# Performance work log

Hardware: AMD Instinct MI355X
Metric: run time of the kernel (lower is better)

Reference implementation:

```python
import jax, jax.numpy as jnp
import numpy as np

D_MODEL = 1024
NUM_HEADS = 16
HEAD_DIM = D_MODEL // NUM_HEADS
B, S = 2, 2048
EPS = 1e-8


def setup_inputs() -> dict:
    key = jax.random.key(0)
    ks = jax.random.split(key, 9)
    sc = 1.0 / np.sqrt(D_MODEL)
    return {
        "x": jax.random.normal(ks[0], (B, S, D_MODEL), jnp.float32),
        "wq": jax.random.normal(ks[1], (D_MODEL, D_MODEL), jnp.float32) * sc,
        "bq": jax.random.normal(ks[2], (D_MODEL,), jnp.float32) * 0.01,
        "wk": jax.random.normal(ks[3], (D_MODEL, D_MODEL), jnp.float32) * sc,
        "bk": jax.random.normal(ks[4], (D_MODEL,), jnp.float32) * 0.01,
        "wv": jax.random.normal(ks[5], (D_MODEL, D_MODEL), jnp.float32) * sc,
        "bv": jax.random.normal(ks[6], (D_MODEL,), jnp.float32) * 0.01,
        "wo": jax.random.normal(ks[7], (D_MODEL, D_MODEL), jnp.float32) * sc,
        "bo": jax.random.normal(ks[8], (D_MODEL,), jnp.float32) * 0.01,
    }


def reference(x, wq, bq, wk, bk, wv, bv, wo, bo):
    b, s, d = x.shape
    h, hd = NUM_HEADS, HEAD_DIM
    # projections (torch Linear: y = x W^T + b); reshape to [b, h, s, hd]
    def proj(w, bias):
        return (jnp.einsum('bsd,ed->bse', x, w) + bias).reshape(b, s, h, hd).transpose(0, 2, 1, 3)
    q = proj(wq, bq)
    k = proj(wk, bk)
    v = proj(wv, bv)
    scores = jnp.einsum('bhqd,bhkd->bhqk', q, k) / np.sqrt(hd)
    attn = jax.nn.softmax(scores, axis=-1)
    o = jnp.einsum('bhqk,bhkd->bhqd', attn, v)  # [b, h, s, hd]
    # per-position, per-head Gram-Schmidt exclusion: remove component of o[i]
    # along v[i] (the loop in the original is independent over positions)
    v_norm_sq = jnp.sum(v * v, axis=-1, keepdims=True)          # [b,h,s,1]
    align = jnp.sum(o * v, axis=-1, keepdims=True) / (v_norm_sq + EPS)
    o = o - align * v
    o = o.transpose(0, 2, 1, 3).reshape(b, s, d)
    return jnp.einsum('bsd,ed->bse', o, wo) + bo
```

## Files before the change

kernel.cpp:

```cpp
#include <hip/hip_runtime.h>
#include <stdint.h>

#define SEQ 2048
#define NTOK 4096
#define DM 1024

typedef __bf16 bf16x8 __attribute__((ext_vector_type(8)));
typedef __bf16 bf16x4 __attribute__((ext_vector_type(4)));
typedef float f32x4 __attribute__((ext_vector_type(4)));

__device__ __forceinline__ unsigned short f2bf(float f) {
  union { float f; unsigned u; } v; v.f = f;
  return (unsigned short)((v.u + 0x7fffu + ((v.u >> 16) & 1u)) >> 16);
}
__device__ __forceinline__ float bf2f(unsigned short s) {
  union { unsigned u; float f; } v; v.u = ((unsigned)s) << 16; return v.f;
}
__device__ __forceinline__ unsigned pkbf(float a, float b) {
  union { float f; unsigned u; } x, y; x.f = a; y.f = b;
  return __builtin_amdgcn_perm(y.u + 0x8000u, x.u + 0x8000u, 0x07060302u);
}

__device__ __forceinline__ void async16(const unsigned short* g, unsigned short* l) {
  __builtin_amdgcn_global_load_lds(
      (const __attribute__((address_space(1))) void*)g,
      (__attribute__((address_space(3))) void*)l, 16, 0, 0);
}

__global__ __launch_bounds__(256) void cast_all(
    const float* __restrict__ x, const float* __restrict__ wq,
    const float* __restrict__ wk, const float* __restrict__ wv,
    const float* __restrict__ wo, unsigned short* __restrict__ dst) {
  size_t i = ((size_t)blockIdx.x * 256 + threadIdx.x) * 4;
  const float* src; size_t off;
  if (i < (size_t)NTOK * DM) { src = x; off = i; }
  else {
    size_t j = i - (size_t)NTOK * DM;
    int s = (int)(j >> 20);
    src = (s == 0) ? wq : (s == 1) ? wk : (s == 2) ? wv : wo;
    off = j & 1048575u;
  }
  float4 f = *(const float4*)(src + off);
  ushort4 o;
  o.x = f2bf(f.x); o.y = f2bf(f.y); o.z = f2bf(f.z); o.w = f2bf(f.w);
  *(ushort4*)(dst + i) = o;
}

__device__ __forceinline__ void gemm128_bk64(
    const unsigned short* __restrict__ A, const unsigned short* __restrict__ Bw,
    int m0, int n0, f32x4 acc[4][4], unsigned short* As, unsigned short* Bs) {
  const int tid = threadIdx.x, lane = tid & 63, w = tid >> 6;
  const int wm = (w >> 1) * 64, wn = (w & 1) * 64;
  const int quad = lane >> 4, l16 = lane & 15, sel = l16 & 7;
  const int srow = tid >> 3;
  const int sc = ((tid & 7) ^ (srow & 7)) << 3;

  for (int kt = 0; kt < 1024; kt += 64) {
    __syncthreads();
#pragma unroll
    for (int c = 0; c < 4; ++c) {
      const int row = c * 32 + srow;
      async16(A + (size_t)(m0 + row) * 1024 + kt + sc, As + c * 2048 + tid * 8);
      async16(Bw + (size_t)(n0 + row) * 1024 + kt + sc, Bs + c * 2048 + tid * 8);
    }
    __syncthreads();
#pragma unroll
    for (int ks = 0; ks < 2; ++ks) {
      bf16x8 af[4], bf[4];
#pragma unroll
      for (int i = 0; i < 4; ++i)
        af[i] = *(const bf16x8*)(As + (wm + i * 16 + l16) * 64 + (((ks * 4 + quad) ^ sel) << 3));
#pragma unroll
      for (int j = 0; j < 4; ++j)
        bf[j] = *(const bf16x8*)(Bs + (wn + j * 16 + l16) * 64 + (((ks * 4 + quad) ^ sel) << 3));
#pragma unroll
      for (int i = 0; i < 4; ++i)
#pragma unroll
        for (int j = 0; j < 4; ++j)
          acc[i][j] = __builtin_amdgcn_mfma_f32_16x16x32_bf16(af[i], bf[j], acc[i][j], 0, 0, 0);
    }
  }
}

__global__ __launch_bounds__(256) void qkv_gemm(
    const unsigned short* __restrict__ xb,
    const unsigned short* __restrict__ wqb, const unsigned short* __restrict__ wkb,
    const unsigned short* __restrict__ wvb,
    const float* __restrict__ bq, const float* __restrict__ bk, const float* __restrict__ bv,
    unsigned short* __restrict__ Q, unsigned short* __restrict__ Kd,
    unsigned short* __restrict__ Vt) {
  __shared__ unsigned short As[128 * 64], Bs[128 * 64];
  const int gx = blockIdx.x;
  const int kind = gx >> 8;
  const int rr = gx & 255;
  const int tok = 4 * (rr & 7) + ((rr >> 3) & 3);
  const int oth = rr >> 5;
  const unsigned short* A; const unsigned short* Bw;
  int m0, n0;
  if (kind == 2) { A = wvb; Bw = xb; m0 = oth * 128; n0 = tok * 128; }
  else { A = xb; Bw = kind ? wkb : wqb; m0 = tok * 128; n0 = oth * 128; }

  f32x4 acc[4][4];
#pragma unroll
  for (int i = 0; i < 4; ++i)
#pragma unroll
    for (int j = 0; j < 4; ++j) { f32x4 z = {0.f, 0.f, 0.f, 0.f}; acc[i][j] = z; }
  gemm128_bk64(A, Bw, m0, n0, acc, As, Bs);

  const int lane = threadIdx.x & 63, w = threadIdx.x >> 6;
  const int quad = lane >> 4, l16 = lane & 15;
  const int wm = (w >> 1) * 64, wn = (w & 1) * 64;

  if (kind == 2) {
#pragma unroll
    for (int i = 0; i < 4; ++i)
#pragma unroll
      for (int j = 0; j < 4; ++j) {
        const int n = n0 + wn + j * 16 + l16;
        const int tb = n >> 11, s = n & 2047;
#pragma unroll
        for (int r = 0; r < 4; ++r) {
          const int m = m0 + wm + i * 16 + quad * 4 + r;
          const int h = m >> 6, d = m & 63;
          Vt[((size_t)(tb * 16 + h) * 64 + d) * SEQ + s] = f2bf(acc[i][j][r] + bv[m]);
        }
      }
  } else {
    const float* bias = (kind == 0) ? bq : bk;
    const float scale = (kind == 0) ? 0.180336880f : 1.0f;
#pragma unroll
    for (int i = 0; i < 4; ++i)
#pragma unroll
      for (int j = 0; j < 4; ++j) {
        const int col = n0 + wn + j * 16 + l16;
        const float bb = bias[col];
        const int h = col >> 6, d = col & 63;
#pragma unroll
        for (int r = 0; r < 4; ++r) {
          const int m = m0 + wm + i * 16 + quad * 4 + r;
          const int b = m >> 11, s = m & 2047;
          const int bh = b * 16 + h;
          const unsigned short val = f2bf((acc[i][j][r] + bb) * scale);
          if (kind == 0) Q[((size_t)bh * SEQ + s) * 64 + d] = val;
          else           Kd[((size_t)bh * SEQ + s) * 64 + d] = val;
        }
      }
  }
}

__global__ __launch_bounds__(256, 2) void attn_kernel(
    const unsigned short* __restrict__ Q, const unsigned short* __restrict__ Kd,
    const unsigned short* __restrict__ Vt,
    unsigned short* __restrict__ Op, float* __restrict__ Lp) {
  __shared__ unsigned short KV[4][4096];
  const int gx = blockIdx.x;
  const int xcd = gx & 7;
  const int idx = gx >> 3;
  const int bh  = xcd * 4 + (idx & 3);
  const int ksl = (idx >> 2) & 1;
  const int q0  = (idx >> 3) * 256;
  const int ks0 = ksl << 10;
  const int tid = threadIdx.x, lane = tid & 63, w = tid >> 6;
  const int quad = lane >> 4, l16 = lane & 15;
  const unsigned short* Qp = Q + (size_t)bh * SEQ * 64;
  const unsigned short* Kp = Kd + (size_t)bh * SEQ * 64;
  const unsigned short* Vp = Vt + (size_t)bh * 64 * SEQ;
  const int srow = tid >> 3;
  const int sc = ((tid & 7) ^ (srow & 7)) << 3;

#pragma unroll
  for (int c = 0; c < 8; ++c)
    async16(Qp + (size_t)(q0 + c * 32 + srow) * 64 + sc,
            KV[c >> 1] + (c & 1) * 2048 + tid * 8);
  __syncthreads();

  const int sel = l16 & 7;
  const unsigned short* Qsrc = KV[w];
  bf16x8 bQ[4][2];
#pragma unroll
  for (int qq = 0; qq < 4; ++qq) {
    const int qrow = qq * 16 + l16;
#pragma unroll
    for (int hh = 0; hh < 2; ++hh)
      bQ[qq][hh] = *(const bf16x8*)(Qsrc + qrow * 64 + (((hh * 4 + quad) ^ sel) << 3));
  }
  __syncthreads();

  async16(Kp + (size_t)(ks0 + srow) * 64 + sc, KV[0] + tid * 8);
  async16(Kp + (size_t)(ks0 + 32 + srow) * 64 + sc, KV[0] + 2048 + tid * 8);
  async16(Vp + (size_t)srow * SEQ + ks0 + sc, KV[2] + tid * 8);
  async16(Vp + (size_t)(32 + srow) * SEQ + ks0 + sc, KV[2] + 2048 + tid * 8);

  union { unsigned short u[8]; bf16x8 v; } one8;
#pragma unroll
  for (int t = 0; t < 8; ++t) one8.u[t] = 0x3F80;
  const bf16x8 aOnes = one8.v;

  f32x4 o_acc[4][4];
  f32x4 l_acc[4];
  const f32x4 zinit = {-12.f, -12.f, -12.f, -12.f};
#pragma unroll
  for (int qq = 0; qq < 4; ++qq) {
    f32x4 z = {0.f, 0.f, 0.f, 0.f};
    l_acc[qq] = z;
#pragma unroll
    for (int dt = 0; dt < 4; ++dt) o_acc[qq][dt] = z;
  }

  for (int it = 0; it < 16; ++it) {
    const int cur = it & 1;
    __syncthreads();
    if (it + 1 < 16) {
      const int kt = ks0 + (it + 1) * 64, nb = (it + 1) & 1;
      async16(Kp + (size_t)(kt + srow) * 64 + sc, KV[nb] + tid * 8);
      async16(Kp + (size_t)(kt + 32 + srow) * 64 + sc, KV[nb] + 2048 + tid * 8);
      async16(Vp + (size_t)srow * SEQ + kt + sc, KV[2 + nb] + tid * 8);
      async16(Vp + (size_t)(32 + srow) * SEQ + kt + sc, KV[2 + nb] + 2048 + tid * 8);
    }
    const unsigned short* Ks = KV[cur];
    const unsigned short* Vs = KV[2 + cur];

    bf16x8 bP[4][2];
#pragma unroll
    for (int kk = 0; kk < 4; ++kk) {
      const int krow = kk * 16 + l16;
      bf16x8 a0 = *(const bf16x8*)(Ks + krow * 64 + ((quad ^ sel) << 3));
      bf16x8 a1 = *(const bf16x8*)(Ks + krow * 64 + (((4 + quad) ^ sel) << 3));
#pragma unroll
      for (int qq = 0; qq < 4; ++qq) {
        f32x4 z = __builtin_amdgcn_mfma_f32_16x16x32_bf16(a0, bQ[qq][0], zinit, 0, 0, 0);
        z = __builtin_amdgcn_mfma_f32_16x16x32_bf16(a1, bQ[qq][1], z, 0, 0, 0);
#pragma unroll
        for (int r = 0; r < 4; ++r) z[r] = __builtin_amdgcn_exp2f(z[r]);
        unsigned lo = pkbf(z[0], z[1]);
        unsigned hi = pkbf(z[2], z[3]);
        union { unsigned d[4]; bf16x8 v; } pk;
        pk.v = bP[qq][kk >> 1];
        pk.d[(kk & 1) * 2] = lo;
        pk.d[(kk & 1) * 2 + 1] = hi;
        bP[qq][kk >> 1] = pk.v;
      }
    }

#pragma unroll
    for (int qq = 0; qq < 4; ++qq)
#pragma unroll
      for (int G = 0; G < 2; ++G)
        l_acc[qq] = __builtin_amdgcn_mfma_f32_16x16x32_bf16(aOnes, bP[qq][G], l_acc[qq], 0, 0, 0);

#pragma unroll
    for (int dt = 0; dt < 4; ++dt) {
      const unsigned short* vbase = Vs + (dt * 16 + l16) * 64;
      const int inner = (quad & 1) * 4;
#pragma unroll
      for (int G = 0; G < 2; ++G) {
        const int c0 = 4 * G + (quad >> 1);
        bf16x4 lo = *(const bf16x4*)(vbase + ((c0 ^ sel) << 3) + inner);
        bf16x4 hi = *(const bf16x4*)(vbase + (((c0 + 2) ^ sel) << 3) + inner);
        bf16x8 aV = __builtin_shufflevector(lo, hi, 0, 1, 2, 3, 4, 5, 6, 7);
#pragma unroll
        for (int qq = 0; qq < 4; ++qq)
          o_acc[qq][dt] = __builtin_amdgcn_mfma_f32_16x16x32_bf16(aV, bP[qq][G], o_acc[qq][dt], 0, 0, 0);
      }
    }
  }

  const size_t sb = (size_t)(ksl * 32 + bh);
#pragma unroll
  for (int qq = 0; qq < 4; ++qq) {
    const int qg = q0 + w * 64 + qq * 16 + l16;
#pragma unroll
    for (int dt = 0; dt < 4; ++dt)
#pragma unroll
      for (int r = 0; r < 4; ++r) {
        const int d = dt * 16 + quad * 4 + r;
        Op[(sb * 64 + d) * SEQ + qg] = f2bf(o_acc[qq][dt][r]);
      }
    if (quad == 0) Lp[sb * SEQ + qg] = l_acc[qq][0];
  }
}

__global__ __launch_bounds__(128) void combine_kernel(
    const unsigned short* __restrict__ Op, const float* __restrict__ Lp,
    const unsigned short* __restrict__ Vt, unsigned short* __restrict__ O) {
  const int bh = blockIdx.y;
  const int q = blockIdx.x * 128 + threadIdx.x;
  const size_t QC = (size_t)32 * SEQ;
  const size_t idx = (size_t)bh * SEQ + q;
  const float inv = 1.0f / (Lp[idx] + Lp[QC + idx]);
  const unsigned short* O1 = Op + (size_t)bh * 64 * SEQ + q;
  const unsigned short* O2 = O1 + QC * 64;
  const unsigned short* Vp = Vt + (size_t)bh * 64 * SEQ + q;
  float o64[64];
  float ov = 0.f, vv = 0.f;
#pragma unroll
  for (int d = 0; d < 64; ++d) {
    const float o = (bf2f(O1[(size_t)d * SEQ]) + bf2f(O2[(size_t)d * SEQ])) * inv;
    const float v = bf2f(Vp[(size_t)d * SEQ]);
    o64[d] = o; ov += o * v; vv += v * v;
  }
  const float align = ov / (vv + 1e-8f);
  const int b = bh >> 4, h = bh & 15;
  unsigned short* dst = O + (size_t)(b * SEQ + q) * DM + h * 64;
#pragma unroll
  for (int d = 0; d < 64; d += 2) {
    const float a0 = o64[d]     - align * bf2f(Vp[(size_t)d * SEQ]);
    const float a1 = o64[d + 1] - align * bf2f(Vp[(size_t)(d + 1) * SEQ]);
    *(unsigned*)(dst + d) = pkbf(a0, a1);
  }
}

__global__ __launch_bounds__(256) void out_gemm(
    const unsigned short* __restrict__ Ob, const unsigned short* __restrict__ wob,
    const float* __restrict__ bo, float* __restrict__ out) {
  __shared__ unsigned short As[64 * 64], Bs[128 * 64];
  const int m0 = blockIdx.y * 64, n0 = blockIdx.x * 128;
  const int tid = threadIdx.x, lane = tid & 63, w = tid >> 6;
  const int wm = (w >> 1) * 32, wn = (w & 1) * 64;
  const int quad = lane >> 4, l16 = lane & 15, sel = l16 & 7;
  const int srow = tid >> 3;
  const int sc = ((tid & 7) ^ (srow & 7)) << 3;
  f32x4 acc[2][4];
#pragma unroll
  for (int i = 0; i < 2; ++i)
#pragma unroll
    for (int j = 0; j < 4; ++j) { f32x4 z = {0.f, 0.f, 0.f, 0.f}; acc[i][j] = z; }

  for (int kt = 0; kt < 1024; kt += 64) {
    __syncthreads();
#pragma unroll
    for (int c = 0; c < 2; ++c) {
      const int row = c * 32 + srow;
      async16(Ob + (size_t)(m0 + row) * 1024 + kt + sc, As + c * 2048 + tid * 8);
    }
#pragma unroll
    for (int c = 0; c < 4; ++c) {
      const int row = c * 32 + srow;
      async16(wob + (size_t)(n0 + row) * 1024 + kt + sc, Bs + c * 2048 + tid * 8);
    }
    __syncthreads();
#pragma unroll
    for (int ks = 0; ks < 2; ++ks) {
      bf16x8 af[2], bf[4];
#pragma unroll
      for (int i = 0; i < 2; ++i)
        af[i] = *(const bf16x8*)(As + (wm + i * 16 + l16) * 64 + (((ks * 4 + quad) ^ sel) << 3));
#pragma unroll
      for (int j = 0; j < 4; ++j)
        bf[j] = *(const bf16x8*)(Bs + (wn + j * 16 + l16) * 64 + (((ks * 4 + quad) ^ sel) << 3));
#pragma unroll
      for (int i = 0; i < 2; ++i)
#pragma unroll
        for (int j = 0; j < 4; ++j)
          acc[i][j] = __builtin_amdgcn_mfma_f32_16x16x32_bf16(af[i], bf[j], acc[i][j], 0, 0, 0);
    }
  }

#pragma unroll
  for (int i = 0; i < 2; ++i)
#pragma unroll
    for (int j = 0; j < 4; ++j) {
      const int col = n0 + wn + j * 16 + l16;
      const float bb = bo[col];
#pragma unroll
      for (int r = 0; r < 4; ++r) {
        const int m = m0 + wm + i * 16 + quad * 4 + r;
        out[(size_t)m * DM + col] = acc[i][j][r] + bb;
      }
    }
}

extern "C" void kernel_launch(void* const* d_in, const int* in_sizes, int n_in,
                              void* d_out, int out_size, void* d_ws, size_t ws_size,
                              hipStream_t stream) {
  const float* x  = (const float*)d_in[0];
  const float* wq = (const float*)d_in[1];
  const float* bq = (const float*)d_in[2];
  const float* wk = (const float*)d_in[3];
  const float* bk = (const float*)d_in[4];
  const float* wv = (const float*)d_in[5];
  const float* bv = (const float*)d_in[6];
  const float* wo = (const float*)d_in[7];
  const float* bo = (const float*)d_in[8];
  float* out = (float*)d_out;
  (void)in_sizes; (void)n_in; (void)out_size; (void)ws_size;

  unsigned short* ws  = (unsigned short*)d_ws;
  unsigned short* xb  = ws;
  unsigned short* wqb = xb + (size_t)NTOK * DM;
  unsigned short* wkb = wqb + (size_t)DM * DM;
  unsigned short* wvb = wkb + (size_t)DM * DM;
  unsigned short* wob = wvb + (size_t)DM * DM;
  unsigned short* Qb  = wob + (size_t)DM * DM;
  unsigned short* Kb  = Qb + (size_t)NTOK * DM;
  unsigned short* Vtb = Kb + (size_t)NTOK * DM;
  unsigned short* Ob  = Vtb + (size_t)NTOK * DM;
  unsigned short* Opb = Ob + (size_t)NTOK * DM;
  float* Lpw = (float*)(Opb + (size_t)2 * 32 * 64 * SEQ);

  cast_all<<<8192, 256, 0, stream>>>(x, wq, wk, wv, wo, ws);
  qkv_gemm<<<768, 256, 0, stream>>>(xb, wqb, wkb, wvb, bq, bk, bv, Qb, Kb, Vtb);
  attn_kernel<<<512, 256, 0, stream>>>(Qb, Kb, Vtb, Opb, Lpw);
  combine_kernel<<<dim3(16, 32), 128, 0, stream>>>(Opb, Lpw, Vtb, Ob);
  out_gemm<<<dim3(8, 64), 256, 0, stream>>>(Ob, wob, bo, out);
}
```

Before: 194.1 us.

## Triple-buffer GEMM LDS tiles with async prefetch and vmcnt-gated barriers

Replaces the synchronous load-then-compute loop in the QKV and output GEMMs with a shared templated pipeline. It uses a 3-slot LDS ring of BK=32 half-tiles and prefetches two stages ahead with global_load_lds. Each step waits on a partial vmcnt before a single barrier, so the next tiles load while MFMAs run. This is meant to hide global memory latency and halve the barrier count per k-step. The cost is more LDS use and hand-tuned waitcnt values that must match the number of issued loads, which is fragile.

Result: faster. 185.7 us (-4.3%).

```diff
diff --git a/kernel.cpp b/kernel.cpp
--- a/kernel.cpp
+++ b/kernel.cpp
@@ -46,50 +46,91 @@
   *(ushort4*)(dst + i) = o;
 }
 
-__device__ __forceinline__ void gemm128_bk64(
+
+template<int MI>
+__device__ __forceinline__ void stage_half(
     const unsigned short* __restrict__ A, const unsigned short* __restrict__ Bw,
-    int m0, int n0, f32x4 acc[4][4], unsigned short* As, unsigned short* Bs) {
+    int m0, int n0, int kt, unsigned short* As, unsigned short* Bs) {
+  const int tid = threadIdx.x;
+  const int r = tid >> 2, c = tid & 3;
+#pragma unroll
+  for (int b = 0; b < MI / 2; ++b) {
+    const int row = b * 64 + r;
+    async16(A + (size_t)(m0 + row) * 1024 + kt + ((c ^ (row & 3)) << 3),
+            As + row * 32 + c * 8);
+  }
+#pragma unroll
+  for (int b = 0; b < 2; ++b) {
+    const int row = b * 64 + r;
+    async16(Bw + (size_t)(n0 + row) * 1024 + kt + ((c ^ (row & 3)) << 3),
+            Bs + row * 32 + c * 8);
+  }
+}
+
+__device__ __forceinline__ void pipe_bar0() {
+  asm volatile("s_waitcnt vmcnt(0)\ns_barrier" ::: "memory");
+}
+template<int MI>
+__device__ __forceinline__ void pipe_barN() {
+  if constexpr (MI == 4) asm volatile("s_waitcnt vmcnt(4)\ns_barrier" ::: "memory");
+  else                   asm volatile("s_waitcnt vmcnt(3)\ns_barrier" ::: "memory");
+}
+
+template<int MI>
+__device__ __forceinline__ void gemm_pipe(
+    const unsigned short* __restrict__ A, const unsigned short* __restrict__ Bw,
+    int m0, int n0, f32x4 (&acc)[MI][4],
+    unsigned short* AsBase, unsigned short* BsBase) {
   const int tid = threadIdx.x, lane = tid & 63, w = tid >> 6;
-  const int wm = (w >> 1) * 64, wn = (w & 1) * 64;
-  const int quad = lane >> 4, l16 = lane & 15, sel = l16 & 7;
-  const int srow = tid >> 3;
-  const int sc = ((tid & 7) ^ (srow & 7)) << 3;
-
-  for (int kt = 0; kt < 1024; kt += 64) {
-    __syncthreads();
-#pragma unroll
-    for (int c = 0; c < 4; ++c) {
-      const int row = c * 32 + srow;
-      async16(A + (size_t)(m0 + row) * 1024 + kt + sc, As + c * 2048 + tid * 8);
-      async16(Bw + (size_t)(n0 + row) * 1024 + kt + sc, Bs + c * 2048 + tid * 8);
+  const int wm16 = (w >> 1) * MI * 16, wn = (w & 1) * 64;
+  const int quad = lane >> 4, l16 = lane & 15;
+  constexpr int ASZ = MI * 32 * 32;
+  constexpr int BSZ = 128 * 32;
+
+  stage_half<MI>(A, Bw, m0, n0, 0,  AsBase,       BsBase);
+  stage_half<MI>(A, Bw, m0, n0, 32, AsBase + ASZ, BsBase + BSZ);
+  pipe_barN<MI>();
+
+  int cur = 0;
+  for (int p = 0; p < 32; ++p) {
+    const unsigned short* As = AsBase + cur * ASZ;
+    const unsigned short* Bs = BsBase + cur * BSZ;
+
+    bf16x8 af[MI], bf[4];
+    const int swz = ((quad ^ (l16 & 3)) << 3);
+#pragma unroll
+    for (int i = 0; i < MI; ++i)
+      af[i] = *(const bf16x8*)(As + (wm16 + i * 16 + l16) * 32 + swz);
+#pragma unroll
+    for (int j = 0; j < 4; ++j)
+      bf[j] = *(const bf16x8*)(Bs + (wn + j * 16 + l16) * 32 + swz);
+
+    if (p + 2 < 32) {
+      const int slot = (cur == 0) ? 2 : cur - 1;
+      stage_half<MI>(A, Bw, m0, n0, (p + 2) * 32,
+                     AsBase + slot * ASZ, BsBase + slot * BSZ);
     }
-    __syncthreads();
-#pragma unroll
-    for (int ks = 0; ks < 2; ++ks) {
-      bf16x8 af[4], bf[4];
-#pragma unroll
-      for (int i = 0; i < 4; ++i)
-        af[i] = *(const bf16x8*)(As + (wm + i * 16 + l16) * 64 + (((ks * 4 + quad) ^ sel) << 3));
+
+#pragma unroll
+    for (int i = 0; i < MI; ++i)
 #pragma unroll
       for (int j = 0; j < 4; ++j)
-        bf[j] = *(const bf16x8*)(Bs + (wn + j * 16 + l16) * 64 + (((ks * 4 + quad) ^ sel) << 3));
-#pragma unroll
-      for (int i = 0; i < 4; ++i)
-#pragma unroll
-        for (int j = 0; j < 4; ++j)
-          acc[i][j] = __builtin_amdgcn_mfma_f32_16x16x32_bf16(af[i], bf[j], acc[i][j], 0, 0, 0);
-    }
-  }
-}
-
-__global__ __launch_bounds__(256) void qkv_gemm(
+        acc[i][j] = __builtin_amdgcn_mfma_f32_16x16x32_bf16(af[i], bf[j], acc[i][j], 0, 0, 0);
+
+    if (p < 30)       pipe_barN<MI>();
+    else if (p == 30) pipe_bar0();
+    cur = (cur == 2) ? 0 : cur + 1;
+  }
+}
+
+__global__ __launch_bounds__(256, 3) void qkv_gemm(
     const unsigned short* __restrict__ xb,
     const unsigned short* __restrict__ wqb, const unsigned short* __restrict__ wkb,
     const unsigned short* __restrict__ wvb,
     const float* __restrict__ bq, const float* __restrict__ bk, const float* __restrict__ bv,
     unsigned short* __restrict__ Q, unsigned short* __restrict__ Kd,
     unsigned short* __restrict__ Vt) {
-  __shared__ unsigned short As[128 * 64], Bs[128 * 64];
+  __shared__ unsigned short As[3 * 128 * 32], Bs[3 * 128 * 32];
   const int gx = blockIdx.x;
   const int kind = gx >> 8;
   const int rr = gx & 255;
@@ -105,7 +146,7 @@
   for (int i = 0; i < 4; ++i)
 #pragma unroll
     for (int j = 0; j < 4; ++j) { f32x4 z = {0.f, 0.f, 0.f, 0.f}; acc[i][j] = z; }
-  gemm128_bk64(A, Bw, m0, n0, acc, As, Bs);
+  gemm_pipe<4>(A, Bw, m0, n0, acc, As, Bs);
 
   const int lane = threadIdx.x & 63, w = threadIdx.x >> 6;
   const int quad = lane >> 4, l16 = lane & 15;
@@ -313,49 +354,19 @@
 __global__ __launch_bounds__(256) void out_gemm(
     const unsigned short* __restrict__ Ob, const unsigned short* __restrict__ wob,
     const float* __restrict__ bo, float* __restrict__ out) {
-  __shared__ unsigned short As[64 * 64], Bs[128 * 64];
+  __shared__ unsigned short As[3 * 64 * 32], Bs[3 * 128 * 32];
   const int m0 = blockIdx.y * 64, n0 = blockIdx.x * 128;
-  const int tid = threadIdx.x, lane = tid & 63, w = tid >> 6;
+  f32x4 acc[2][4];
+#pragma unroll
+  for (int i = 0; i < 2; ++i)
+#pragma unroll
+    for (int j = 0; j < 4; ++j) { f32x4 z = {0.f, 0.f, 0.f, 0.f}; acc[i][j] = z; }
+
+  gemm_pipe<2>(Ob, wob, m0, n0, acc, As, Bs);
+
+  const int lane = threadIdx.x & 63, w = threadIdx.x >> 6;
+  const int quad = lane >> 4, l16 = lane & 15;
   const int wm = (w >> 1) * 32, wn = (w & 1) * 64;
-  const int quad = lane >> 4, l16 = lane & 15, sel = l16 & 7;
-  const int srow = tid >> 3;
-  const int sc = ((tid & 7) ^ (srow & 7)) << 3;
-  f32x4 acc[2][4];
-#pragma unroll
-  for (int i = 0; i < 2; ++i)
-#pragma unroll
-    for (int j = 0; j < 4; ++j) { f32x4 z = {0.f, 0.f, 0.f, 0.f}; acc[i][j] = z; }
-
-  for (int kt = 0; kt < 1024; kt += 64) {
-    __syncthreads();
-#pragma unroll
-    for (int c = 0; c < 2; ++c) {
-      const int row = c * 32 + srow;
-      async16(Ob + (size_t)(m0 + row) * 1024 + kt + sc, As + c * 2048 + tid * 8);
-    }
-#pragma unroll
-    for (int c = 0; c < 4; ++c) {
-      const int row = c * 32 + srow;
-      async16(wob + (size_t)(n0 + row) * 1024 + kt + sc, Bs + c * 2048 + tid * 8);
-    }
-    __syncthreads();
-#pragma unroll
-    for (int ks = 0; ks < 2; ++ks) {
-      bf16x8 af[2], bf[4];
-#pragma unroll
-      for (int i = 0; i < 2; ++i)
-        af[i] = *(const bf16x8*)(As + (wm + i * 16 + l16) * 64 + (((ks * 4 + quad) ^ sel) << 3));
-#pragma unroll
-      for (int j = 0; j < 4; ++j)
-        bf[j] = *(const bf16x8*)(Bs + (wn + j * 16 + l16) * 64 + (((ks * 4 + quad) ^ sel) << 3));
-#pragma unroll
-      for (int i = 0; i < 2; ++i)
-#pragma unroll
-        for (int j = 0; j < 4; ++j)
-          acc[i][j] = __builtin_amdgcn_mfma_f32_16x16x32_bf16(af[i], bf[j], acc[i][j], 0, 0, 0);
-    }
-  }
-
 #pragma unroll
   for (int i = 0; i < 2; ++i)
 #pragma unroll
```
